# Optimization experiments

Measured on AMD Instinct MI355X. Metric: run time of the kernel, lower is better.

Reference implementation:

```python
import jax, jax.numpy as jnp
import numpy as np

B, S, D = 4, 2048, 1024


def setup_inputs() -> dict:
    key = jax.random.key(0)
    ks = jax.random.split(key, 9)
    scale = 1.0 / np.sqrt(D)
    x = jax.random.normal(ks[0], (B, S, D), dtype=jnp.float32)
    # causal mask (batch, seq, seq), int32; positions with 0 are masked out
    mask = jnp.broadcast_to(jnp.tril(jnp.ones((S, S), dtype=jnp.int32)), (B, S, S))
    Wq = jax.random.uniform(ks[1], (D, D), jnp.float32, -scale, scale)
    bq = jax.random.uniform(ks[2], (D,), jnp.float32, -scale, scale)
    Wk = jax.random.uniform(ks[3], (D, D), jnp.float32, -scale, scale)
    bk = jax.random.uniform(ks[4], (D,), jnp.float32, -scale, scale)
    Wv = jax.random.uniform(ks[5], (D, D), jnp.float32, -scale, scale)
    bv = jax.random.uniform(ks[6], (D,), jnp.float32, -scale, scale)
    Wo = jax.random.uniform(ks[7], (D, D), jnp.float32, -scale, scale)
    bo = jax.random.uniform(ks[8], (D,), jnp.float32, -scale, scale)
    return {"x": x, "mask": mask, "Wq": Wq, "bq": bq, "Wk": Wk, "bk": bk,
            "Wv": Wv, "bv": bv, "Wo": Wo, "bo": bo}


def reference(x, mask, Wq, bq, Wk, bk, Wv, bv, Wo, bo):
    d_model = x.shape[-1]
    scaling = jnp.sqrt(jnp.asarray(d_model, dtype=jnp.float32))
    # torch nn.Linear: y = x @ W.T + b
    Q = jnp.einsum('bsd,ed->bse', x, Wq) + bq
    K = jnp.einsum('bsd,ed->bse', x, Wk) + bk
    V = jnp.einsum('bsd,ed->bse', x, Wv) + bv
    scores = jnp.einsum('bqd,bkd->bqk', Q, K) / scaling  # (B, S, S)
    scores = jnp.where(mask == 0, jnp.float32(-1e9), scores)
    attn = jax.nn.softmax(scores, axis=2)
    out = jnp.einsum('bqk,bkd->bqd', attn, V)
    out = jnp.einsum('bsd,ed->bse', out, Wo) + bo
    return out, attn
```

## Files before the change

kernel.cpp:

```cpp
#include <hip/hip_runtime.h>
#include <hip/hip_bf16.h>
#include <stdint.h>


typedef unsigned short u16;
typedef __attribute__((ext_vector_type(8))) __bf16 bf16x8;
typedef __attribute__((ext_vector_type(8))) unsigned short u16x8;
typedef __attribute__((ext_vector_type(4))) float f32x4;

__device__ __forceinline__ u16 f2bf(float f) {
  unsigned int u = __builtin_bit_cast(unsigned int, f);
  u = u + 0x7FFFu + ((u >> 16) & 1u);
  return (u16)(u >> 16);
}

__device__ __forceinline__ float bf2f(u16 u) {
  unsigned int w = ((unsigned int)u) << 16;
  return __builtin_bit_cast(float, w);
}

__device__ __forceinline__ void gl_lds16(const void* g, void* l) {
  __builtin_amdgcn_global_load_lds(
      (const __attribute__((address_space(1))) void*)g,
      (__attribute__((address_space(3))) void*)l, 16, 0, 0);
}

#define MFMA(a, b, c) __builtin_amdgcn_mfma_f32_16x16x32_bf16((a), (b), (c), 0, 0, 0)

#define TILE 128
#define BKK  64
template<int GM, int GX, int OUTMODE, bool BIAS, bool CKB, int NTT>
__global__ __launch_bounds__(256) void gemm_bt(
    const u16* __restrict__ A, const u16* __restrict__ Bmat,
    const float* __restrict__ b0, const float* __restrict__ b1,
    const float* __restrict__ b2,
    void* __restrict__ C0, u16* __restrict__ C1, u16* __restrict__ C2,
    int N, int K, long long sAb, long long sBb, long long sCb, int nchunk) {
  __shared__ __align__(16) u16 As[2][TILE * BKK];
  __shared__ __align__(16) u16 Bs[2][TILE * BKK];
  const int bid = blockIdx.x;

  if (GM == 7 && bid >= 544) {
    const int tt_ = threadIdx.x;
    const int v = bid - 544;
    const int bz2 = v >> 7, dt = (v >> 4) & 7, st = v & 15;
    const u16* src = C1 + (size_t)bz2 * 2097152 + (size_t)st * 131072 + dt * 128;
    u16* dst2 = C2 + (size_t)bz2 * 2097152 + (size_t)dt * 262144 + st * 128;
    u16* T = (u16*)As;
    const int c8 = tt_ & 15, qd = tt_ >> 4;
#pragma unroll
    for (int pass = 0; pass < 2; ++pass) {
      const int s0 = pass * 64 + qd * 4;
      u16x8 r[4];
#pragma unroll
      for (int i = 0; i < 4; ++i)
        r[i] = *(const u16x8*)(src + (size_t)(s0 + i) * 1024 + c8 * 8);
#pragma unroll
      for (int j = 0; j < 8; ++j) {
        const int col = c8 * 8 + j;
        ushort4 q;
        q.x = r[0][j]; q.y = r[1][j]; q.z = r[2][j]; q.w = r[3][j];
        *(ushort4*)((char*)T + col * 256 +
                    ((s0 * 2) ^ ((j ^ (c8 & 7)) << 4))) = q;
      }
    }
    __syncthreads();
#pragma unroll
    for (int it = 0; it < 8; ++it) {
      const int lin = it * 256 + tt_;
      const int d = lin >> 4, ch = lin & 15;
      u16x8 w = *(const u16x8*)((const char*)T + d * 256 + ch * 16);
      const int che = ch ^ (d & 7) ^ ((d >> 3) & 7);
      *(u16x8*)(dst2 + (size_t)d * 2048 + che * 8) = w;
    }
    return;
  }

  int bx, by, bz;
  if (GM == 1 || GM == 7) {
    const int lidx = (bid & 7) * nchunk + (bid >> 3);
    bz = lidx / 136;
    const int i = lidx - bz * 136;
    by = (int)((sqrtf(8.f * i + 1.f) - 1.f) * 0.5f);
    while ((by + 1) * (by + 2) / 2 <= i) ++by;
    while (by * (by + 1) / 2 > i) --by;
    bx = i - by * (by + 1) / 2;
  } else if (GM == 3) {
    const int j = bid & 255;
    const int k = j >> 5;
    by = (bid >> 8) ? k : 15 - k;
    bz = (j & 31) >> 3;
    bx = j & 7;
  } else {
    const int xcd = bid & 7, c = bid >> 3;
    bz = 0;
    by = xcd * 8 + (c >> 3);
    bx = c & 7;
  }
  const int t = threadIdx.x;
  const int lane = t & 63, wid = t >> 6;
  const int wm = (wid >> 1) * 64, wn = (wid & 1) * 64;
  const int fr = lane & 15, fh = lane >> 4;

  const char* Ab = (const char*)(A + (size_t)bz * sAb + (size_t)by * TILE * K);
  const size_t rowstride = (size_t)K * 2;
  const size_t BOFF = (size_t)8 * TILE * rowstride;
  const char* Btile = (const char*)(Bmat + (size_t)bz * sBb + (size_t)bx * TILE * K);

  int srow[4], scol[4], slin[4];
#pragma unroll
  for (int c = 0; c < 4; ++c) {
    slin[c] = c * 4096 + t * 16;
    srow[c] = slin[c] >> 7;
    scol[c] = (slin[c] & 127) ^ ((srow[c] & 7) << 4);
  }

  int Keff = K;
  if (CKB) { int kb2 = (by + 1) * TILE; Keff = kb2 < K ? kb2 : K; }
  const int nkt = Keff / BKK;

#define STAGE(ko_, buf_, Bp_)                                                 \
  {                                                                           \
    _Pragma("unroll") for (int c = 0; c < 4; ++c) {                           \
      gl_lds16(Ab + (size_t)srow[c] * rowstride + (ko_) + scol[c],            \
               (char*)As[buf_] + slin[c]);                                    \
      gl_lds16((Bp_) + (size_t)srow[c] * rowstride + (ko_) + scol[c],         \
               (char*)Bs[buf_] + slin[c]);                                    \
    }                                                                         \
  }

  STAGE(0, 0, Btile)
  __syncthreads();

  int cur = 0;
  for (int tt = 0; tt < NTT; ++tt) {
    f32x4 acc[4][4];
#pragma unroll
    for (int m = 0; m < 4; ++m)
#pragma unroll
      for (int n = 0; n < 4; ++n) acc[m][n] = {0.f, 0.f, 0.f, 0.f};

    for (int kt = 0; kt < nkt; ++kt) {
      const bool last = (kt + 1 == nkt);
      if (!last) {
        STAGE((size_t)(kt + 1) * (BKK * 2), cur ^ 1, Btile)
      } else if (NTT > 1 && tt + 1 < NTT) {
        STAGE(0, cur ^ 1, Btile + BOFF)
      }
      const char* Ac = (const char*)As[cur];
      const char* Bc = (const char*)Bs[cur];
#pragma unroll
      for (int kk = 0; kk < BKK; kk += 32) {
        bf16x8 af[4], bg[4];
#pragma unroll
        for (int m = 0; m < 4; ++m) {
          int r = wm + m * 16 + fr;
          int cb = (kk * 2 + fh * 16) ^ ((r & 7) << 4);
          af[m] = *(const bf16x8*)(Ac + r * 128 + cb);
        }
#pragma unroll
        for (int n = 0; n < 4; ++n) {
          int r = wn + n * 16 + fr;
          int cb = (kk * 2 + fh * 16) ^ ((r & 7) << 4);
          bg[n] = *(const bf16x8*)(Bc + r * 128 + cb);
        }
#pragma unroll
        for (int m = 0; m < 4; ++m)
#pragma unroll
          for (int n = 0; n < 4; ++n)
            acc[m][n] = MFMA(af[m], bg[n], acc[m][n]);
      }
      if (!last) __syncthreads();
      cur ^= 1;
    }

    const int bxe = bx + 8 * tt;
    const int gm0 = by * TILE + wm, gn0 = bxe * TILE + wn;
#pragma unroll
    for (int n = 0; n < 4; ++n) {
      const int gc = gn0 + n * 16 + fr;
      float bvv = 0.f;
      if (BIAS) {
        if (OUTMODE == 3) {
          const int w = bxe >> 3;
          bvv = (w == 0 ? b0 : w == 1 ? b1 : b2)[gc & 1023];
        } else {
          bvv = b0[gc];
        }
      }
#pragma unroll
      for (int m = 0; m < 4; ++m) {
        const int gr0 = gm0 + m * 16 + fh * 4;
        float v[4];
#pragma unroll
        for (int j = 0; j < 4; ++j) v[j] = acc[m][n][j] + bvv;
        if (OUTMODE == 1) {
          float* C = (float*)C0 + (size_t)bz * sCb;
#pragma unroll
          for (int j = 0; j < 4; ++j) C[(size_t)(gr0 + j) * N + gc] = v[j];
        } else if (OUTMODE == 0) {
          u16* C = (u16*)C0 + (size_t)bz * sCb;
#pragma unroll
          for (int j = 0; j < 4; ++j) C[(size_t)(gr0 + j) * N + gc] = f2bf(v[j]);
        } else {
          const int w = bxe >> 3;
          const int gcl = gc & 1023;
          u16* dst = (w == 0) ? (u16*)C0 : (w == 1) ? C1 : C2;
          const float sc = (w == 0) ? 0.03125f : 1.0f;
#pragma unroll
          for (int j = 0; j < 4; ++j)
            dst[(size_t)(gr0 + j) * 1024 + gcl] = f2bf(v[j] * sc);
        }
      }
    }

    if (NTT > 1 && tt + 1 < NTT) {
      __syncthreads();
      Btile += BOFF;
    }
  }
#undef STAGE
}

__global__ __launch_bounds__(256) void cvt_w(
    const float4* __restrict__ wq, const float4* __restrict__ wk,
    const float4* __restrict__ wo, const float* __restrict__ wv_f,
    const float* __restrict__ bv, ushort4* __restrict__ wqb,
    ushort4* __restrict__ wkb, ushort4* __restrict__ wob,
    u16* __restrict__ wvtb, float* __restrict__ bvo,
    const float* __restrict__ wo_f) {
  __shared__ __align__(16) u16 T[128 * 136];
  const int bid = blockIdx.x, t = threadIdx.x;
  if (bid < 3072) {
    const int w = bid >> 10;
    const int idx = (bid & 1023) * 256 + t;
    const float4* s = (w == 0) ? wq : (w == 1) ? wk : wo;
    ushort4* d = (w == 0) ? wqb : (w == 1) ? wkb : wob;
    float4 v = s[idx];
    ushort4 o;
    o.x = f2bf(v.x); o.y = f2bf(v.y); o.z = f2bf(v.z); o.w = f2bf(v.w);
    d[idx] = o;
  } else if (bid < 3136) {
    const int bb = bid - 3072;
    const int ti = bb >> 3, tj = bb & 7;
#pragma unroll
    for (int it = 0; it < 16; ++it) {
      const int lin = it * 256 + t;
      const int r = lin >> 5, c4 = lin & 31;
      float4 v = *(const float4*)(wv_f + (size_t)(tj * 128 + r) * 1024 +
                                  ti * 128 + c4 * 4);
      T[(c4 * 4 + 0) * 136 + r] = f2bf(v.x);
      T[(c4 * 4 + 1) * 136 + r] = f2bf(v.y);
      T[(c4 * 4 + 2) * 136 + r] = f2bf(v.z);
      T[(c4 * 4 + 3) * 136 + r] = f2bf(v.w);
    }
    __syncthreads();
#pragma unroll
    for (int it = 0; it < 8; ++it) {
      const int lin = it * 256 + t;
      const int il = lin >> 4, ch = lin & 15;
      bf16x8 v = *(const bf16x8*)((const char*)T + il * 272 + ch * 16);
      *(bf16x8*)((char*)wvtb + (size_t)(ti * 128 + il) * 2048 + tj * 256 +
                 ch * 16) = v;
    }
  } else {
    float* bvs = (float*)T;
#pragma unroll
    for (int k = 0; k < 4; ++k) bvs[k * 256 + t] = bv[k * 256 + t];
    __syncthreads();
    const int e = (bid - 3136) * 256 + t;
    float a = 0.f;
    const float* wr = wo_f + (size_t)e * 1024;
#pragma unroll 8
    for (int d = 0; d < 1024; ++d) a += wr[d] * bvs[d];
    bvo[e] = a;
  }
}

__global__ __launch_bounds__(256) void prep2(
    const u16* __restrict__ wob, const u16* __restrict__ wvtb,
    u16* __restrict__ wvob, const float4* __restrict__ x,
    ushort4* __restrict__ xb) {
  __shared__ __align__(16) u16 As[2][8192];
  __shared__ __align__(16) u16 Bs[2][8192];
  const int bid = blockIdx.x;
  const int t = threadIdx.x;
  if (bid >= 64) {
    const int i = (bid - 64) * 256 + t;
    float4 v = x[i];
    ushort4 o;
    o.x = f2bf(v.x); o.y = f2bf(v.y); o.z = f2bf(v.z); o.w = f2bf(v.w);
    xb[i] = o;
    return;
  }
  const int by = bid >> 3, bx = bid & 7;
  const int lane = t & 63, wid = t >> 6;
  const int wm = (wid >> 1) * 64, wn = (wid & 1) * 64;
  const int fr = lane & 15, fh = lane >> 4;
  const char* Ab = (const char*)(wob + (size_t)by * 128 * 1024);
  const char* Bb = (const char*)(wvtb + (size_t)bx * 128 * 1024);
  int srow[4], scol[4], slin[4];
#pragma unroll
  for (int c = 0; c < 4; ++c) {
    slin[c] = c * 4096 + t * 16;
    srow[c] = slin[c] >> 7;
    scol[c] = (slin[c] & 127) ^ ((srow[c] & 7) << 4);
  }
#define STG2(ko_, buf_)                                                       \
  {                                                                           \
    _Pragma("unroll") for (int c = 0; c < 4; ++c) {                           \
      gl_lds16(Ab + (size_t)srow[c] * 2048 + (ko_) + scol[c],                 \
               (char*)As[buf_] + slin[c]);                                    \
      gl_lds16(Bb + (size_t)srow[c] * 2048 + (ko_) + scol[c],                 \
               (char*)Bs[buf_] + slin[c]);                                    \
    }                                                                         \
  }
  STG2(0, 0)
  __syncthreads();
  f32x4 acc[4][4];
#pragma unroll
  for (int m = 0; m < 4; ++m)
#pragma unroll
    for (int n = 0; n < 4; ++n) acc[m][n] = {0.f, 0.f, 0.f, 0.f};
  int cur = 0;
  for (int kt = 0; kt < 16; ++kt) {
    const bool last = (kt == 15);
    if (!last) STG2((size_t)(kt + 1) * 128, cur ^ 1)
    const char* Ac = (const char*)As[cur];
    const char* Bc = (const char*)Bs[cur];
#pragma unroll
    for (int kk = 0; kk < 64; kk += 32) {
      bf16x8 af[4], bg[4];
#pragma unroll
      for (int m = 0; m < 4; ++m) {
        int r = wm + m * 16 + fr;
        int cb = (kk * 2 + fh * 16) ^ ((r & 7) << 4);
        af[m] = *(const bf16x8*)(Ac + r * 128 + cb);
      }
#pragma unroll
      for (int n = 0; n < 4; ++n) {
        int r = wn + n * 16 + fr;
        int cb = (kk * 2 + fh * 16) ^ ((r & 7) << 4);
        bg[n] = *(const bf16x8*)(Bc + r * 128 + cb);
      }
#pragma unroll
      for (int m = 0; m < 4; ++m)
#pragma unroll
        for (int n = 0; n < 4; ++n)
          acc[m][n] = MFMA(af[m], bg[n], acc[m][n]);
    }
    if (!last) __syncthreads();
    cur ^= 1;
  }
  const int gm0 = by * 128 + wm, gn0 = bx * 128 + wn;
#pragma unroll
  for (int n = 0; n < 4; ++n) {
    const int gc = gn0 + n * 16 + fr;
#pragma unroll
    for (int m = 0; m < 4; ++m) {
      const int gr0 = gm0 + m * 16 + fh * 4;
#pragma unroll
      for (int j = 0; j < 4; ++j)
        wvob[(size_t)(gr0 + j) * 1024 + gc] = f2bf(acc[m][n][j]);
    }
  }
#undef STG2
}

__global__ __launch_bounds__(256) void softmax_rows(
    u16* __restrict__ pb, float* __restrict__ attnF) {
  const int row = blockIdx.x;
  const int q = row & 2047;
  const int nv = q + 1;
  const int nvt = (q & ~127) + 128;
  const int t = threadIdx.x;
  u16* brow = pb + (size_t)row * 2048;
  float* srow = attnF + (size_t)row * 2048;
  __shared__ float red[4];

  const int e0 = 8 * t;
  float a[8];
  if (e0 < nvt) {
    ushort4 u0 = ((const ushort4*)brow)[2 * t];
    ushort4 u1 = ((const ushort4*)brow)[2 * t + 1];
    u16 us[8] = {u0.x, u0.y, u0.z, u0.w, u1.x, u1.y, u1.z, u1.w};
#pragma unroll
    for (int j = 0; j < 8; ++j)
      a[j] = (e0 + j < nv) ? bf2f(us[j]) : -3.0e38f;
  } else {
#pragma unroll
    for (int j = 0; j < 8; ++j) a[j] = -3.0e38f;
  }

  float lmax = -3.0e38f;
#pragma unroll
  for (int j = 0; j < 8; ++j) lmax = fmaxf(lmax, a[j]);
#pragma unroll
  for (int o = 32; o > 0; o >>= 1) lmax = fmaxf(lmax, __shfl_xor(lmax, o));
  if ((t & 63) == 0) red[t >> 6] = lmax;
  __syncthreads();
  const float m = fmaxf(fmaxf(red[0], red[1]), fmaxf(red[2], red[3]));
  __syncthreads();

  float lsum = 0.f;
#pragma unroll
  for (int j = 0; j < 8; ++j) {
    a[j] = __expf(a[j] - m);
    lsum += a[j];
  }
#pragma unroll
  for (int o = 32; o > 0; o >>= 1) lsum += __shfl_xor(lsum, o);
  if ((t & 63) == 0) red[t >> 6] = lsum;
  __syncthreads();
  const float inv = 1.f / (red[0] + red[1] + red[2] + red[3]);

#pragma unroll
  for (int j = 0; j < 8; ++j) a[j] *= inv;
  ((float4*)srow)[2 * t]     = float4{a[0], a[1], a[2], a[3]};
  ((float4*)srow)[2 * t + 1] = float4{a[4], a[5], a[6], a[7]};
  if (e0 < nvt) {
    ushort4 ba; ba.x = f2bf(a[0]); ba.y = f2bf(a[1]); ba.z = f2bf(a[2]); ba.w = f2bf(a[3]);
    ushort4 bb; bb.x = f2bf(a[4]); bb.y = f2bf(a[5]); bb.z = f2bf(a[6]); bb.w = f2bf(a[7]);
    ((ushort4*)brow)[2 * t]     = ba;
    ((ushort4*)brow)[2 * t + 1] = bb;
  }
}

extern "C" void kernel_launch(void* const* d_in, const int* in_sizes, int n_in,
                              void* d_out, int out_size, void* d_ws,
                              size_t ws_size, hipStream_t stream) {
  (void)in_sizes; (void)n_in; (void)out_size; (void)ws_size;
  const int B = 4, S = 2048, D = 1024;
  const float* x  = (const float*)d_in[0];
  const float* Wq = (const float*)d_in[2]; const float* bq = (const float*)d_in[3];
  const float* Wk = (const float*)d_in[4]; const float* bk = (const float*)d_in[5];
  const float* Wv = (const float*)d_in[6]; const float* bv = (const float*)d_in[7];
  const float* Wo = (const float*)d_in[8]; const float* bo = (const float*)d_in[9];

  float* out  = (float*)d_out;
  float* attn = out + (size_t)B * S * D;

  char* ws = (char*)d_ws;
  u16* xb   = (u16*)(ws);
  u16* wqb  = (u16*)(ws + 16777216);
  u16* wkb  = wqb + 1048576;
  u16* wvob = wkb + 1048576;
  u16* wob  = wvob + 1048576;
  u16* qb   = (u16*)(ws + 25165824);
  u16* kb   = (u16*)(ws + 41943040);
  u16* vr   = (u16*)(ws + 58720256);
  u16* pb   = (u16*)(ws + 75497472);
  u16* wvtb = pb;
  float* bvo = (float*)(ws + 75497472 + 2097152);

  cvt_w<<<3140, 256, 0, stream>>>(
      (const float4*)Wq, (const float4*)Wk, (const float4*)Wo, Wv, bv,
      (ushort4*)wqb, (ushort4*)wkb, (ushort4*)wob, wvtb, bvo, Wo);

  prep2<<<8256, 256, 0, stream>>>(wob, wvtb, wvob, (const float4*)x,
                                  (ushort4*)xb);

  gemm_bt<4, 24, 3, true, false, 3><<<512, 256, 0, stream>>>(
      xb, wqb, bq, bk, bvo, qb, kb, vr, 3072, 1024, 0, 0, 0, 0);

  gemm_bt<7, 1, 0, false, false, 1><<<1056, 256, 0, stream>>>(
      qb, kb, nullptr, nullptr, nullptr, pb, vr, xb,
      2048, 1024, (long long)S * D, (long long)S * D, (long long)S * S, 68);

  softmax_rows<<<B * S, 256, 0, stream>>>(pb, attn);

  gemm_bt<3, 8, 1, true, true, 1><<<512, 256, 0, stream>>>(
      pb, xb, bo, nullptr, nullptr, out, nullptr, nullptr,
      1024, 2048, (long long)S * S, (long long)D * S, (long long)S * D, 0);
}
```

Before: 224.7 us.

## Fold Wq and Wk into a combined Wq^T Wk projection to drop the K GEMM

```diff
diff --git a/kernel.cpp b/kernel.cpp
--- a/kernel.cpp
+++ b/kernel.cpp
@@ -39,74 +39,11 @@
   __shared__ __align__(16) u16 As[2][TILE * BKK];
   __shared__ __align__(16) u16 Bs[2][TILE * BKK];
   const int bid = blockIdx.x;
-
-  if (GM == 7 && bid >= 544) {
-    const int tt_ = threadIdx.x;
-    const int v = bid - 544;
-    const int bz2 = v >> 7, dt = (v >> 4) & 7, st = v & 15;
-    const u16* src = C1 + (size_t)bz2 * 2097152 + (size_t)st * 131072 + dt * 128;
-    u16* dst2 = C2 + (size_t)bz2 * 2097152 + (size_t)dt * 262144 + st * 128;
-    u16* T = (u16*)As;
-    const int c8 = tt_ & 15, qd = tt_ >> 4;
-#pragma unroll
-    for (int pass = 0; pass < 2; ++pass) {
-      const int s0 = pass * 64 + qd * 4;
-      u16x8 r[4];
-#pragma unroll
-      for (int i = 0; i < 4; ++i)
-        r[i] = *(const u16x8*)(src + (size_t)(s0 + i) * 1024 + c8 * 8);
-#pragma unroll
-      for (int j = 0; j < 8; ++j) {
-        const int col = c8 * 8 + j;
-        ushort4 q;
-        q.x = r[0][j]; q.y = r[1][j]; q.z = r[2][j]; q.w = r[3][j];
-        *(ushort4*)((char*)T + col * 256 +
-                    ((s0 * 2) ^ ((j ^ (c8 & 7)) << 4))) = q;
-      }
-    }
-    __syncthreads();
-#pragma unroll
-    for (int it = 0; it < 8; ++it) {
-      const int lin = it * 256 + tt_;
-      const int d = lin >> 4, ch = lin & 15;
-      u16x8 w = *(const u16x8*)((const char*)T + d * 256 + ch * 16);
-      const int che = ch ^ (d & 7) ^ ((d >> 3) & 7);
-      *(u16x8*)(dst2 + (size_t)d * 2048 + che * 8) = w;
-    }
-    return;
-  }
-
-  int bx, by, bz;
-  if (GM == 1 || GM == 7) {
-    const int lidx = (bid & 7) * nchunk + (bid >> 3);
-    bz = lidx / 136;
-    const int i = lidx - bz * 136;
-    by = (int)((sqrtf(8.f * i + 1.f) - 1.f) * 0.5f);
-    while ((by + 1) * (by + 2) / 2 <= i) ++by;
-    while (by * (by + 1) / 2 > i) --by;
-    bx = i - by * (by + 1) / 2;
-  } else if (GM == 3) {
-    const int j = bid & 255;
-    const int k = j >> 5;
-    by = (bid >> 8) ? k : 15 - k;
-    bz = (j & 31) >> 3;
-    bx = j & 7;
-  } else {
-    const int xcd = bid & 7, c = bid >> 3;
-    bz = 0;
-    by = xcd * 8 + (c >> 3);
-    bx = c & 7;
-  }
   const int t = threadIdx.x;
   const int lane = t & 63, wid = t >> 6;
   const int wm = (wid >> 1) * 64, wn = (wid & 1) * 64;
   const int fr = lane & 15, fh = lane >> 4;
 
-  const char* Ab = (const char*)(A + (size_t)bz * sAb + (size_t)by * TILE * K);
-  const size_t rowstride = (size_t)K * 2;
-  const size_t BOFF = (size_t)8 * TILE * rowstride;
-  const char* Btile = (const char*)(Bmat + (size_t)bz * sBb + (size_t)bx * TILE * K);
-
   int srow[4], scol[4], slin[4];
 #pragma unroll
   for (int c = 0; c < 4; ++c) {
@@ -115,9 +52,40 @@
     scol[c] = (slin[c] & 127) ^ ((srow[c] & 7) << 4);
   }
 
-  int Keff = K;
-  if (CKB) { int kb2 = (by + 1) * TILE; Keff = kb2 < K ? kb2 : K; }
-  const int nkt = Keff / BKK;
+  const int lidx0 = (bid & 7) * 64 + (bid >> 3);
+  const int nrep = (GM == 8) ? (((lidx0 & 15) == 0) ? 2 : 1) : 1;
+
+  for (int rep = 0; rep < nrep; ++rep) {
+    int bx, by, bz;
+    if (GM == 3) {
+      const int j = bid & 255;
+      const int k = j >> 5;
+      by = (bid >> 8) ? k : 15 - k;
+      bz = (j & 31) >> 3;
+      bx = j & 7;
+    } else if (GM == 4) {
+      const int xcd = bid & 7, c = bid >> 3;
+      bz = 0;
+      by = xcd * 8 + (c >> 3);
+      bx = c & 7;
+    } else {
+      int lidx = (rep == 0) ? lidx0 : 512 + (lidx0 >> 4);
+      bz = lidx / 136;
+      const int i = lidx - bz * 136;
+      by = (int)((sqrtf(8.f * i + 1.f) - 1.f) * 0.5f);
+      while ((by + 1) * (by + 2) / 2 <= i) ++by;
+      while (by * (by + 1) / 2 > i) --by;
+      bx = i - by * (by + 1) / 2;
+    }
+
+    const char* Ab = (const char*)(A + (size_t)bz * sAb + (size_t)by * TILE * K);
+    const size_t rowstride = (size_t)K * 2;
+    const size_t BOFF = (size_t)8 * TILE * rowstride;
+    const char* Btile = (const char*)(Bmat + (size_t)bz * sBb + (size_t)bx * TILE * K);
+
+    int Keff = K;
+    if (CKB) { int kb2 = (by + 1) * TILE; Keff = kb2 < K ? kb2 : K; }
+    const int nkt = Keff / BKK;
 
 #define STAGE(ko_, buf_, Bp_)                                                 \
   {                                                                           \
@@ -129,125 +97,130 @@
     }                                                                         \
   }
 
-  STAGE(0, 0, Btile)
-  __syncthreads();
-
-  int cur = 0;
-  for (int tt = 0; tt < NTT; ++tt) {
-    f32x4 acc[4][4];
-#pragma unroll
-    for (int m = 0; m < 4; ++m)
-#pragma unroll
-      for (int n = 0; n < 4; ++n) acc[m][n] = {0.f, 0.f, 0.f, 0.f};
-
-    for (int kt = 0; kt < nkt; ++kt) {
-      const bool last = (kt + 1 == nkt);
-      if (!last) {
-        STAGE((size_t)(kt + 1) * (BKK * 2), cur ^ 1, Btile)
-      } else if (NTT > 1 && tt + 1 < NTT) {
-        STAGE(0, cur ^ 1, Btile + BOFF)
-      }
-      const char* Ac = (const char*)As[cur];
-      const char* Bc = (const char*)Bs[cur];
-#pragma unroll
-      for (int kk = 0; kk < BKK; kk += 32) {
-        bf16x8 af[4], bg[4];
+    if (GM == 8 && rep) __syncthreads();
+    STAGE(0, 0, Btile)
+    __syncthreads();
+
+    int cur = 0;
+    const char* Bt = Btile;
+    for (int tt = 0; tt < NTT; ++tt) {
+      f32x4 acc[4][4];
+#pragma unroll
+      for (int m = 0; m < 4; ++m)
+#pragma unroll
+        for (int n = 0; n < 4; ++n) acc[m][n] = {0.f, 0.f, 0.f, 0.f};
+
+      for (int kt = 0; kt < nkt; ++kt) {
+        const bool last = (kt + 1 == nkt);
+        if (!last) {
+          STAGE((size_t)(kt + 1) * (BKK * 2), cur ^ 1, Bt)
+        } else if (NTT > 1 && tt + 1 < NTT) {
+          STAGE(0, cur ^ 1, Bt + BOFF)
+        }
+        const char* Ac = (const char*)As[cur];
+        const char* Bc = (const char*)Bs[cur];
+#pragma unroll
+        for (int kk = 0; kk < BKK; kk += 32) {
+          bf16x8 af[4], bg[4];
+#pragma unroll
+          for (int m = 0; m < 4; ++m) {
+            int r = wm + m * 16 + fr;
+            int cb = (kk * 2 + fh * 16) ^ ((r & 7) << 4);
+            af[m] = *(const bf16x8*)(Ac + r * 128 + cb);
+          }
+#pragma unroll
+          for (int n = 0; n < 4; ++n) {
+            int r = wn + n * 16 + fr;
+            int cb = (kk * 2 + fh * 16) ^ ((r & 7) << 4);
+            bg[n] = *(const bf16x8*)(Bc + r * 128 + cb);
+          }
+#pragma unroll
+          for (int m = 0; m < 4; ++m)
+#pragma unroll
+            for (int n = 0; n < 4; ++n)
+              acc[m][n] = MFMA(af[m], bg[n], acc[m][n]);
+        }
+        if (!last) __syncthreads();
+        cur ^= 1;
+      }
+
+      const int bxe = bx + 8 * tt;
+      const int gm0 = by * TILE + wm, gn0 = bxe * TILE + wn;
+#pragma unroll
+      for (int n = 0; n < 4; ++n) {
+        const int gc = gn0 + n * 16 + fr;
+        float badd = 0.f;
+        if (OUTMODE == 1 && BIAS) badd = b0[gc];
+        if (OUTMODE == 4) badd = b1[bz * 2048 + gc] + b2[0];
+        if (OUTMODE == 3 && (bxe >> 3) == 1) badd = b2[gc & 1023];
 #pragma unroll
         for (int m = 0; m < 4; ++m) {
-          int r = wm + m * 16 + fr;
-          int cb = (kk * 2 + fh * 16) ^ ((r & 7) << 4);
-          af[m] = *(const bf16x8*)(Ac + r * 128 + cb);
+          const int gr0 = gm0 + m * 16 + fh * 4;
+          if (OUTMODE == 1) {
+            float* C = (float*)C0 + (size_t)bz * sCb;
+#pragma unroll
+            for (int j = 0; j < 4; ++j)
+              C[(size_t)(gr0 + j) * N + gc] = acc[m][n][j] + badd;
+          } else if (OUTMODE == 4) {
+            u16* C = (u16*)C0 + (size_t)bz * sCb;
+#pragma unroll
+            for (int j = 0; j < 4; ++j)
+              C[(size_t)(gr0 + j) * N + gc] =
+                  f2bf(acc[m][n][j] + badd + b0[bz * 2048 + gr0 + j]);
+          } else {
+            const int gcl = gc & 1023;
+            u16* dst = ((bxe >> 3) == 0) ? (u16*)C0 : C2;
+#pragma unroll
+            for (int j = 0; j < 4; ++j)
+              dst[(size_t)(gr0 + j) * 1024 + gcl] = f2bf(acc[m][n][j] + badd);
+          }
         }
-#pragma unroll
-        for (int n = 0; n < 4; ++n) {
-          int r = wn + n * 16 + fr;
-          int cb = (kk * 2 + fh * 16) ^ ((r & 7) << 4);
-          bg[n] = *(const bf16x8*)(Bc + r * 128 + cb);
-        }
-#pragma unroll
-        for (int m = 0; m < 4; ++m)
-#pragma unroll
-          for (int n = 0; n < 4; ++n)
-            acc[m][n] = MFMA(af[m], bg[n], acc[m][n]);
-      }
-      if (!last) __syncthreads();
-      cur ^= 1;
-    }
-
-    const int bxe = bx + 8 * tt;
-    const int gm0 = by * TILE + wm, gn0 = bxe * TILE + wn;
-#pragma unroll
-    for (int n = 0; n < 4; ++n) {
-      const int gc = gn0 + n * 16 + fr;
-      float bvv = 0.f;
-      if (BIAS) {
-        if (OUTMODE == 3) {
-          const int w = bxe >> 3;
-          bvv = (w == 0 ? b0 : w == 1 ? b1 : b2)[gc & 1023];
-        } else {
-          bvv = b0[gc];
-        }
-      }
-#pragma unroll
-      for (int m = 0; m < 4; ++m) {
-        const int gr0 = gm0 + m * 16 + fh * 4;
-        float v[4];
-#pragma unroll
-        for (int j = 0; j < 4; ++j) v[j] = acc[m][n][j] + bvv;
-        if (OUTMODE == 1) {
-          float* C = (float*)C0 + (size_t)bz * sCb;
-#pragma unroll
-          for (int j = 0; j < 4; ++j) C[(size_t)(gr0 + j) * N + gc] = v[j];
-        } else if (OUTMODE == 0) {
-          u16* C = (u16*)C0 + (size_t)bz * sCb;
-#pragma unroll
-          for (int j = 0; j < 4; ++j) C[(size_t)(gr0 + j) * N + gc] = f2bf(v[j]);
-        } else {
-          const int w = bxe >> 3;
-          const int gcl = gc & 1023;
-          u16* dst = (w == 0) ? (u16*)C0 : (w == 1) ? C1 : C2;
-          const float sc = (w == 0) ? 0.03125f : 1.0f;
-#pragma unroll
-          for (int j = 0; j < 4; ++j)
-            dst[(size_t)(gr0 + j) * 1024 + gcl] = f2bf(v[j] * sc);
-        }
-      }
-    }
-
-    if (NTT > 1 && tt + 1 < NTT) {
-      __syncthreads();
-      Btile += BOFF;
-    }
-  }
+      }
+
+      if (NTT > 1 && tt + 1 < NTT) {
+        __syncthreads();
+        Bt += BOFF;
+      }
+    }
 #undef STAGE
+  }
 }
 
 __global__ __launch_bounds__(256) void cvt_w(
-    const float4* __restrict__ wq, const float4* __restrict__ wk,
-    const float4* __restrict__ wo, const float* __restrict__ wv_f,
-    const float* __restrict__ bv, ushort4* __restrict__ wqb,
-    ushort4* __restrict__ wkb, ushort4* __restrict__ wob,
-    u16* __restrict__ wvtb, float* __restrict__ bvo,
-    const float* __restrict__ wo_f) {
+    const float4* __restrict__ x4, const float4* __restrict__ wo4,
+    const float* __restrict__ wq_f, const float* __restrict__ wk_f,
+    const float* __restrict__ wv_f, const float* __restrict__ wo_f,
+    const float* __restrict__ bq, const float* __restrict__ bk,
+    const float* __restrict__ bv,
+    ushort4* __restrict__ xb4, ushort4* __restrict__ wob4,
+    u16* __restrict__ wqt, u16* __restrict__ wkt, u16* __restrict__ wvt,
+    float* __restrict__ wqbk, float* __restrict__ wkbq,
+    float* __restrict__ cbuf, float* __restrict__ bvo) {
   __shared__ __align__(16) u16 T[128 * 136];
   const int bid = blockIdx.x, t = threadIdx.x;
-  if (bid < 3072) {
-    const int w = bid >> 10;
-    const int idx = (bid & 1023) * 256 + t;
-    const float4* s = (w == 0) ? wq : (w == 1) ? wk : wo;
-    ushort4* d = (w == 0) ? wqb : (w == 1) ? wkb : wob;
-    float4 v = s[idx];
+  if (bid < 8192) {
+    const int idx = bid * 256 + t;
+    float4 v = x4[idx];
     ushort4 o;
     o.x = f2bf(v.x); o.y = f2bf(v.y); o.z = f2bf(v.z); o.w = f2bf(v.w);
-    d[idx] = o;
-  } else if (bid < 3136) {
-    const int bb = bid - 3072;
-    const int ti = bb >> 3, tj = bb & 7;
+    xb4[idx] = o;
+  } else if (bid < 9216) {
+    const int idx = (bid - 8192) * 256 + t;
+    float4 v = wo4[idx];
+    ushort4 o;
+    o.x = f2bf(v.x); o.y = f2bf(v.y); o.z = f2bf(v.z); o.w = f2bf(v.w);
+    wob4[idx] = o;
+  } else if (bid < 9408) {
+    const int bb = bid - 9216;
+    const int mat = bb >> 6, tl = bb & 63;
+    const int ti = tl >> 3, tj = tl & 7;
+    const float* src = (mat == 0) ? wq_f : (mat == 1) ? wk_f : wv_f;
+    u16* dst = (mat == 0) ? wqt : (mat == 1) ? wkt : wvt;
 #pragma unroll
     for (int it = 0; it < 16; ++it) {
       const int lin = it * 256 + t;
       const int r = lin >> 5, c4 = lin & 31;
-      float4 v = *(const float4*)(wv_f + (size_t)(tj * 128 + r) * 1024 +
+      float4 v = *(const float4*)(src + (size_t)(tj * 128 + r) * 1024 +
                                   ti * 128 + c4 * 4);
       T[(c4 * 4 + 0) * 136 + r] = f2bf(v.x);
       T[(c4 * 4 + 1) * 136 + r] = f2bf(v.y);
@@ -260,45 +233,113 @@
       const int lin = it * 256 + t;
       const int il = lin >> 4, ch = lin & 15;
       bf16x8 v = *(const bf16x8*)((const char*)T + il * 272 + ch * 16);
-      *(bf16x8*)((char*)wvtb + (size_t)(ti * 128 + il) * 2048 + tj * 256 +
+      *(bf16x8*)((char*)dst + (size_t)(ti * 128 + il) * 2048 + tj * 256 +
                  ch * 16) = v;
     }
-  } else {
+  } else if (bid < 9440) {
     float* bvs = (float*)T;
 #pragma unroll
     for (int k = 0; k < 4; ++k) bvs[k * 256 + t] = bv[k * 256 + t];
     __syncthreads();
-    const int e = (bid - 3136) * 256 + t;
-    float a = 0.f;
-    const float* wr = wo_f + (size_t)e * 1024;
+    const int b = bid - 9408;
+    const int lane = t & 63, w = t >> 6;
+    const float4* bv4 = (const float4*)bvs;
+#pragma unroll
+    for (int i = 0; i < 8; ++i) {
+      const int o = b * 32 + w * 8 + i;
+      const float4* wr = (const float4*)(wo_f + (size_t)o * 1024);
+      float s = 0.f;
+#pragma unroll
+      for (int k = 0; k < 4; ++k) {
+        float4 a = wr[lane + 64 * k], bb = bv4[lane + 64 * k];
+        s += a.x * bb.x + a.y * bb.y + a.z * bb.z + a.w * bb.w;
+      }
+#pragma unroll
+      for (int off = 32; off > 0; off >>= 1) s += __shfl_xor(s, off);
+      if (lane == 0) bvo[o] = s;
+    }
+  } else {
+    const int vb = bid - 9440;
+    if (vb < 8) {
+      const float* W = (vb < 4) ? wq_f : wk_f;
+      const float* bvec = (vb < 4) ? bk : bq;
+      float* outp = (vb < 4) ? wqbk : wkbq;
+      float* bl = (float*)T;
+#pragma unroll
+      for (int k = 0; k < 4; ++k) bl[k * 256 + t] = bvec[k * 256 + t];
+      __syncthreads();
+      const int d = (vb & 3) * 256 + t;
+      float a = 0.f;
 #pragma unroll 8
-    for (int d = 0; d < 1024; ++d) a += wr[d] * bvs[d];
-    bvo[e] = a;
+      for (int e = 0; e < 1024; ++e) a += W[(size_t)e * 1024 + d] * bl[e];
+      outp[d] = a * 0.03125f;
+    } else {
+      float p = 0.f;
+#pragma unroll
+      for (int k = 0; k < 4; ++k) p += bq[k * 256 + t] * bk[k * 256 + t];
+      float* rs = (float*)T;
+      rs[t] = p;
+      __syncthreads();
+      for (int off = 128; off > 0; off >>= 1) {
+        if (t < off) rs[t] += rs[t + off];
+        __syncthreads();
+      }
+      if (t == 0) cbuf[0] = rs[0] * 0.03125f;
+    }
   }
 }
 
 __global__ __launch_bounds__(256) void prep2(
-    const u16* __restrict__ wob, const u16* __restrict__ wvtb,
-    u16* __restrict__ wvob, const float4* __restrict__ x,
-    ushort4* __restrict__ xb) {
+    const u16* __restrict__ wkt, const u16* __restrict__ wqt,
+    u16* __restrict__ wqkt, const u16* __restrict__ wob,
+    const u16* __restrict__ wvt, u16* __restrict__ wvob,
+    const u16* __restrict__ xb, const float* __restrict__ wqbk,
+    const float* __restrict__ wkbq, float* __restrict__ uu,
+    float* __restrict__ vv) {
   __shared__ __align__(16) u16 As[2][8192];
   __shared__ __align__(16) u16 Bs[2][8192];
   const int bid = blockIdx.x;
   const int t = threadIdx.x;
-  if (bid >= 64) {
-    const int i = (bid - 64) * 256 + t;
-    float4 v = x[i];
-    ushort4 o;
-    o.x = f2bf(v.x); o.y = f2bf(v.y); o.z = f2bf(v.z); o.w = f2bf(v.w);
-    xb[i] = o;
+  if (bid >= 128) {
+    const int vid = bid - 128;
+    const int kind = vid >> 9, grp = vid & 511;
+    const float* vec = kind ? wkbq : wqbk;
+    float* outp = kind ? vv : uu;
+    float* vl = (float*)As;
+#pragma unroll
+    for (int k = 0; k < 4; ++k) vl[k * 256 + t] = vec[k * 256 + t];
+    __syncthreads();
+    const int lane = t & 63, w = t >> 6;
+#pragma unroll
+    for (int i = 0; i < 4; ++i) {
+      const int r = grp * 16 + w * 4 + i;
+      const u16* xr = xb + (size_t)r * 1024 + lane * 16;
+      bf16x8 h0 = *(const bf16x8*)(xr);
+      bf16x8 h1 = *(const bf16x8*)(xr + 8);
+      float s = 0.f;
+#pragma unroll
+      for (int k = 0; k < 8; ++k) {
+        s += (float)h0[k] * vl[lane * 16 + k];
+        s += (float)h1[k] * vl[lane * 16 + 8 + k];
+      }
+#pragma unroll
+      for (int off = 32; off > 0; off >>= 1) s += __shfl_xor(s, off);
+      if (lane == 0) outp[r] = s;
+    }
     return;
   }
-  const int by = bid >> 3, bx = bid & 7;
+  const int role = bid >> 6;
+  const int b2 = bid & 63;
+  const int by = b2 >> 3, bx = b2 & 7;
+  const float scale = role ? 1.0f : 0.03125f;
+  const u16* Au = role ? wob : wkt;
+  const u16* Bu = role ? wvt : wqt;
+  u16* Cu = role ? wvob : wqkt;
   const int lane = t & 63, wid = t >> 6;
   const int wm = (wid >> 1) * 64, wn = (wid & 1) * 64;
   const int fr = lane & 15, fh = lane >> 4;
-  const char* Ab = (const char*)(wob + (size_t)by * 128 * 1024);
-  const char* Bb = (const char*)(wvtb + (size_t)bx * 128 * 1024);
+  const char* Ab = (const char*)(Au + (size_t)by * 128 * 1024);
+  const char* Bb = (const char*)(Bu + (size_t)bx * 128 * 1024);
   int srow[4], scol[4], slin[4];
 #pragma unroll
   for (int c = 0; c < 4; ++c) {
@@ -361,22 +402,61 @@
       const int gr0 = gm0 + m * 16 + fh * 4;
 #pragma unroll
       for (int j = 0; j < 4; ++j)
-        wvob[(size_t)(gr0 + j) * 1024 + gc] = f2bf(acc[m][n][j]);
+        Cu[(size_t)(gr0 + j) * 1024 + gc] = f2bf(acc[m][n][j] * scale);
     }
   }
 #undef STG2
 }
 
 __global__ __launch_bounds__(256) void softmax_rows(
-    u16* __restrict__ pb, float* __restrict__ attnF) {
-  const int row = blockIdx.x;
+    u16* __restrict__ pb, float* __restrict__ attnF,
+    const u16* __restrict__ vr, u16* __restrict__ vt) {
+  __shared__ __align__(16) u16 shm[16384];
+  const int bid = blockIdx.x;
+  const int t = threadIdx.x;
+
+  if (bid < 512) {
+    const int v = bid;
+    const int bz2 = v >> 7, dt = (v >> 4) & 7, st = v & 15;
+    const u16* src = vr + (size_t)bz2 * 2097152 + (size_t)st * 131072 + dt * 128;
+    u16* dst2 = vt + (size_t)bz2 * 2097152 + (size_t)dt * 262144 + st * 128;
+    u16* T = shm;
+    const int c8 = t & 15, qd = t >> 4;
+#pragma unroll
+    for (int pass = 0; pass < 2; ++pass) {
+      const int s0 = pass * 64 + qd * 4;
+      u16x8 r[4];
+#pragma unroll
+      for (int i = 0; i < 4; ++i)
+        r[i] = *(const u16x8*)(src + (size_t)(s0 + i) * 1024 + c8 * 8);
+#pragma unroll
+      for (int j = 0; j < 8; ++j) {
+        const int col = c8 * 8 + j;
+        ushort4 q;
+        q.x = r[0][j]; q.y = r[1][j]; q.z = r[2][j]; q.w = r[3][j];
+        *(ushort4*)((char*)T + col * 256 +
+                    ((s0 * 2) ^ ((j ^ (c8 & 7)) << 4))) = q;
+      }
+    }
+    __syncthreads();
+#pragma unroll
+    for (int it = 0; it < 8; ++it) {
+      const int lin = it * 256 + t;
+      const int d = lin >> 4, ch = lin & 15;
+      u16x8 w = *(const u16x8*)((const char*)T + d * 256 + ch * 16);
+      const int che = ch ^ (d & 7) ^ ((d >> 3) & 7);
+      *(u16x8*)(dst2 + (size_t)d * 2048 + che * 8) = w;
+    }
+    return;
+  }
+
+  const int row = bid - 512;
   const int q = row & 2047;
   const int nv = q + 1;
   const int nvt = (q & ~127) + 128;
-  const int t = threadIdx.x;
   u16* brow = pb + (size_t)row * 2048;
   float* srow = attnF + (size_t)row * 2048;
-  __shared__ float red[4];
+  float* red = (float*)shm;
 
   const int e0 = 8 * t;
   float a[8];
@@ -441,33 +521,39 @@
   float* attn = out + (size_t)B * S * D;
 
   char* ws = (char*)d_ws;
-  u16* xb   = (u16*)(ws);
-  u16* wqb  = (u16*)(ws + 16777216);
-  u16* wkb  = wqb + 1048576;
-  u16* wvob = wkb + 1048576;
-  u16* wob  = wvob + 1048576;
-  u16* qb   = (u16*)(ws + 25165824);
-  u16* kb   = (u16*)(ws + 41943040);
-  u16* vr   = (u16*)(ws + 58720256);
-  u16* pb   = (u16*)(ws + 75497472);
-  u16* wvtb = pb;
-  float* bvo = (float*)(ws + 75497472 + 2097152);
-
-  cvt_w<<<3140, 256, 0, stream>>>(
-      (const float4*)Wq, (const float4*)Wk, (const float4*)Wo, Wv, bv,
-      (ushort4*)wqb, (ushort4*)wkb, (ushort4*)wob, wvtb, bvo, Wo);
-
-  prep2<<<8256, 256, 0, stream>>>(wob, wvtb, wvob, (const float4*)x,
-                                  (ushort4*)xb);
-
-  gemm_bt<4, 24, 3, true, false, 3><<<512, 256, 0, stream>>>(
-      xb, wqb, bq, bk, bvo, qb, kb, vr, 3072, 1024, 0, 0, 0, 0);
-
-  gemm_bt<7, 1, 0, false, false, 1><<<1056, 256, 0, stream>>>(
-      qb, kb, nullptr, nullptr, nullptr, pb, vr, xb,
-      2048, 1024, (long long)S * D, (long long)S * D, (long long)S * S, 68);
-
-  softmax_rows<<<B * S, 256, 0, stream>>>(pb, attn);
+  u16* xb    = (u16*)(ws);
+  u16* wob   = (u16*)(ws + 16777216);
+  u16* wqt   = (u16*)(ws + 18874368);
+  u16* wkt   = (u16*)(ws + 20971520);
+  u16* wvt   = (u16*)(ws + 23068672);
+  u16* wqkt  = (u16*)(ws + 25165824);
+  u16* wvob  = (u16*)(ws + 27262976);
+  float* wqbk = (float*)(ws + 29360128);
+  float* wkbq = (float*)(ws + 29364224);
+  float* cbuf = (float*)(ws + 29368320);
+  float* bvo  = (float*)(ws + 29372416);
+  float* uu   = (float*)(ws + 29376512);
+  float* vv   = (float*)(ws + 29409280);
+  u16* qb    = (u16*)(ws + 30408704);
+  u16* vr    = (u16*)(ws + 47185920);
+  u16* pb    = (u16*)(ws + 63963136);
+
+  cvt_w<<<9449, 256, 0, stream>>>(
+      (const float4*)x, (const float4*)Wo, Wq, Wk, Wv, Wo, bq, bk, bv,
+      (ushort4*)xb, (ushort4*)wob, wqt, wkt, wvt, wqbk, wkbq, cbuf, bvo);
+
+  prep2<<<1152, 256, 0, stream>>>(wkt, wqt, wqkt, wob, wvt, wvob, xb,
+                                  wqbk, wkbq, uu, vv);
+
+  gemm_bt<4, 0, 3, false, false, 2><<<512, 256, 0, stream>>>(
+      xb, wqkt, nullptr, nullptr, bvo, qb, nullptr, vr,
+      2048, 1024, 0, 0, 0, 0);
+
+  gemm_bt<8, 0, 4, false, false, 1><<<512, 256, 0, stream>>>(
+      qb, xb, uu, vv, cbuf, pb, nullptr, nullptr,
+      2048, 1024, (long long)S * D, (long long)S * D, (long long)S * S, 64);
+
+  softmax_rows<<<8704, 256, 0, stream>>>(pb, attn, vr, xb);
 
   gemm_bt<3, 8, 1, true, true, 1><<<512, 256, 0, stream>>>(
       pb, xb, bo, nullptr, nullptr, out, nullptr, nullptr,
```

After: 232.4 us. +3.4%, slower.
